# Kernel optimization log

Hardware: AMD Instinct MI355X
Metric: run time of the kernel (lower is better)

## Reference

```python
import jax, jax.numpy as jnp
import numpy as np

N_SRC1, N_DST1, N_DST2 = 200000, 50000, 10000
E1, E2 = 2000000, 400000
IN_F, H_F, N_CLS = 128, 256, 47


def setup_inputs() -> dict:
    key = jax.random.key(0)
    ks = jax.random.split(key, 10)
    x = jax.random.normal(ks[0], (N_SRC1, IN_F), dtype=jnp.float32)
    W_self1 = jax.random.normal(ks[1], (IN_F, H_F), dtype=jnp.float32) * (1.0 / np.sqrt(IN_F))
    W_neigh1 = jax.random.normal(ks[2], (IN_F, H_F), dtype=jnp.float32) * (1.0 / np.sqrt(IN_F))
    b1 = jnp.zeros((H_F,), dtype=jnp.float32)
    W_self2 = jax.random.normal(ks[3], (H_F, N_CLS), dtype=jnp.float32) * (1.0 / np.sqrt(H_F))
    W_neigh2 = jax.random.normal(ks[4], (H_F, N_CLS), dtype=jnp.float32) * (1.0 / np.sqrt(H_F))
    b2 = jnp.zeros((N_CLS,), dtype=jnp.float32)
    src1 = jax.random.randint(ks[5], (E1,), 0, N_SRC1, dtype=jnp.int64)
    dst1 = jnp.sort(jax.random.randint(ks[6], (E1,), 0, N_DST1, dtype=jnp.int64))
    src2 = jax.random.randint(ks[7], (E2,), 0, N_DST1, dtype=jnp.int64)
    dst2 = jnp.sort(jax.random.randint(ks[8], (E2,), 0, N_DST2, dtype=jnp.int64))
    return {"x": x, "W_self1": W_self1, "W_neigh1": W_neigh1, "b1": b1,
            "W_self2": W_self2, "W_neigh2": W_neigh2, "b2": b2,
            "src1": src1, "dst1": dst1, "src2": src2, "dst2": dst2,
            "n_dst1": N_DST1, "n_dst2": N_DST2}


def _sage_mean(h_src, h_dst, src, dst, n_dst, W_self, W_neigh, b):
    # mean neighbor aggregation: gather src feats, segment-sum onto dst, divide by in-degree
    msum = jax.ops.segment_sum(h_src[src], dst, num_segments=n_dst)  # [n_dst, F]
    deg = jax.ops.segment_sum(jnp.ones(src.shape, h_src.dtype), dst, num_segments=n_dst)
    h_neigh = msum / jnp.maximum(deg, 1.0)[:, None]
    return h_dst @ W_self + h_neigh @ W_neigh + b


def reference(x, W_self1, W_neigh1, b1, W_self2, W_neigh2, b2,
              src1, dst1, src2, dst2, n_dst1, n_dst2):
    # layer 1 (dst nodes are the prefix of src nodes, DGL MFG convention)
    h = _sage_mean(x, x[:n_dst1], src1, dst1, n_dst1, W_self1, W_neigh1, b1)
    h = jax.nn.relu(h)  # dropout = identity (eval mode)
    # layer 2
    out = _sage_mean(h, h[:n_dst2], src2, dst2, n_dst2, W_self2, W_neigh2, b2)
    return out
```

## Files before the change

### kernel.cpp

```cpp
#include <hip/hip_runtime.h>

constexpr int N_DST1 = 50000;
constexpr int N_DST2 = 10000;
constexpr int E1     = 2000000;
constexpr int E2     = 400000;
constexpr int IN_F   = 128;
constexpr int H_F    = 256;
constexpr int N_CLS  = 47;

constexpr size_t RP1_OFF = 0;
constexpr size_t RP2_OFF = 204800;
constexpr size_t BPS_OFF = 245760;
constexpr size_t BPN_OFF = 311296;
constexpr size_t BP2_OFF = 376832;
constexpr size_t X8_OFF  = 430080;
constexpr size_t HN1_OFF = 26030080;
constexpr size_t HB_OFF  = 38830080;
constexpr size_t H8_OFF  = 64430080;
constexpr size_t HN2_OFF = 77230080;

using f32x4  = __attribute__((ext_vector_type(4))) float;
using f32x2  = __attribute__((ext_vector_type(2))) float;
using short8 = __attribute__((ext_vector_type(8))) short;

__device__ __forceinline__ ushort f2bf(float f) {
    union { float f; unsigned u; } v; v.f = f;
    unsigned u = v.u;
    return (ushort)((u + 0x7fffu + ((u >> 16) & 1u)) >> 16);
}

constexpr int CAST_BLKS = 200000 * IN_F / 8 / 256;
constexpr int PACK_BLKS = 44;
constexpr int RP_BLKS   = (N_DST1 + N_DST2 + 2 + 255) / 256;

__global__ __launch_bounds__(256) void setup_all(
    const float* __restrict__ x, unsigned char* __restrict__ x8,
    const float* __restrict__ Ws1, const float* __restrict__ Wn1,
    const float* __restrict__ Ws2, const float* __restrict__ Wn2,
    ushort* __restrict__ bps, ushort* __restrict__ bpn, ushort* __restrict__ bp2,
    const int* __restrict__ dst1, const int* __restrict__ dst2,
    int* __restrict__ rp1, int* __restrict__ rp2) {
    int b = blockIdx.x;
    if (b < CAST_BLKS) {
        int i = b * 256 + threadIdx.x;
        float4 v0 = ((const float4*)x)[2 * i];
        float4 v1 = ((const float4*)x)[2 * i + 1];
        int p0 = __builtin_amdgcn_cvt_pk_fp8_f32(v0.x, v0.y, 0, false);
        p0     = __builtin_amdgcn_cvt_pk_fp8_f32(v0.z, v0.w, p0, true);
        int p1 = __builtin_amdgcn_cvt_pk_fp8_f32(v1.x, v1.y, 0, false);
        p1     = __builtin_amdgcn_cvt_pk_fp8_f32(v1.z, v1.w, p1, true);
        uint2 o; o.x = (unsigned)p0; o.y = (unsigned)p1;
        ((uint2*)x8)[i] = o;
    } else if (b < CAST_BLKS + PACK_BLKS) {
        int pb = b - CAST_BLKS;
        if (pb < 32) {
            const float* W = (pb < 16) ? Ws1 : Wn1;
            ushort* P      = (pb < 16) ? bps : bpn;
            int idx = (pb & 15) * 256 + threadIdx.x;
            int lane = idx & 63, kb = (idx >> 6) & 3, nb = idx >> 8;
            int n  = nb * 16 + (lane & 15);
            int k0 = kb * 32 + ((lane >> 4) * 8);
            ushort tmp[8];
#pragma unroll
            for (int j = 0; j < 8; ++j) tmp[j] = f2bf(W[(k0 + j) * H_F + n]);
            ((uint4*)P)[idx] = *(uint4*)tmp;
        } else {
            int idx = (pb - 32) * 256 + threadIdx.x;
            if (idx < 3072) {
                int lane = idx & 63, rem = idx >> 6;
                int nb = rem % 3, kb = rem / 3;
                int col = nb * 16 + (lane & 15);
                int k0  = (kb & 7) * 32 + ((lane >> 4) * 8);
                const float* W = (kb < 8) ? Ws2 : Wn2;
                ushort tmp[8];
#pragma unroll
                for (int j = 0; j < 8; ++j)
                    tmp[j] = (col < N_CLS) ? f2bf(W[(k0 + j) * N_CLS + col]) : (ushort)0;
                ((uint4*)bp2)[(kb * 3 + nb) * 64 + lane] = *(uint4*)tmp;
            }
        }
    } else {
        int idx = (b - CAST_BLKS - PACK_BLKS) * 256 + threadIdx.x;
        const int* dst; int* rp; int E; int target;
        if (idx <= N_DST1) { dst = dst1; rp = rp1; E = E1; target = idx; }
        else if (idx <= N_DST1 + 1 + N_DST2) {
            dst = dst2; rp = rp2; E = E2; target = idx - (N_DST1 + 1);
        } else return;
        int lo = 0, hi = E;
        while (lo < hi) {
            int mid = (lo + hi) >> 1;
            if (dst[mid] < target) lo = mid + 1; else hi = mid;
        }
        rp[target] = lo;
    }
}

__global__ __launch_bounds__(256) void agg1b(const unsigned char* __restrict__ x8,
                                             const int* __restrict__ src,
                                             const int* __restrict__ rp,
                                             ushort* __restrict__ hn) {
    int t = threadIdx.x & 63;
    int d = blockIdx.x * 4 + (threadIdx.x >> 6);
    int s = rp[d], e = rp[d + 1];
    int deg = e - s;
    const uint4* x4 = (const uint4*)x8;
    int g = t >> 3, c = t & 7;
    float a[16] = {};
    auto acc16 = [&](uint4 v) {
        f32x2 f;
        f = __builtin_amdgcn_cvt_pk_f32_fp8((int)v.x, false); a[0]  += f[0]; a[1]  += f[1];
        f = __builtin_amdgcn_cvt_pk_f32_fp8((int)v.x, true);  a[2]  += f[0]; a[3]  += f[1];
        f = __builtin_amdgcn_cvt_pk_f32_fp8((int)v.y, false); a[4]  += f[0]; a[5]  += f[1];
        f = __builtin_amdgcn_cvt_pk_f32_fp8((int)v.y, true);  a[6]  += f[0]; a[7]  += f[1];
        f = __builtin_amdgcn_cvt_pk_f32_fp8((int)v.z, false); a[8]  += f[0]; a[9]  += f[1];
        f = __builtin_amdgcn_cvt_pk_f32_fp8((int)v.z, true);  a[10] += f[0]; a[11] += f[1];
        f = __builtin_amdgcn_cvt_pk_f32_fp8((int)v.w, false); a[12] += f[0]; a[13] += f[1];
        f = __builtin_amdgcn_cvt_pk_f32_fp8((int)v.w, true);  a[14] += f[0]; a[15] += f[1];
    };
    int nfull = deg >> 3;
    int j = 0;
    for (; j + 2 <= nfull; j += 2) {
        int e0 = src[s + 8 * j + g];
        int e1 = src[s + 8 * j + 8 + g];
        uint4 v0 = x4[(size_t)e0 * 8 + c];
        uint4 v1 = x4[(size_t)e1 * 8 + c];
        acc16(v0);
        acc16(v1);
    }
    for (; j < nfull; ++j) {
        int e0 = src[s + 8 * j + g];
        uint4 v = x4[(size_t)e0 * 8 + c];
        acc16(v);
    }
    int b0 = s + 8 * nfull;
    int n = e - b0;
    if (g < n) {
        int e0 = src[b0 + g];
        uint4 v = x4[(size_t)e0 * 8 + c];
        acc16(v);
    }
#pragma unroll
    for (int q = 0; q < 16; ++q) {
        a[q] += __shfl_xor(a[q], 8);
        a[q] += __shfl_xor(a[q], 16);
        a[q] += __shfl_xor(a[q], 32);
    }
    if (t < 8) {
        float inv = 1.f / fmaxf((float)deg, 1.f);
        unsigned o[8];
#pragma unroll
        for (int p = 0; p < 8; ++p)
            o[p] = (unsigned)f2bf(a[2 * p] * inv) |
                   ((unsigned)f2bf(a[2 * p + 1] * inv) << 16);
        uint4* hrow = (uint4*)hn + (size_t)d * 16 + t * 2;
        hrow[0] = make_uint4(o[0], o[1], o[2], o[3]);
        hrow[1] = make_uint4(o[4], o[5], o[6], o[7]);
    }
}

__global__ __launch_bounds__(256) void agg2b(const unsigned char* __restrict__ h8,
                                             const int* __restrict__ src,
                                             const int* __restrict__ rp,
                                             ushort* __restrict__ hn) {
    int t = threadIdx.x & 63;
    int d = blockIdx.x * 4 + (threadIdx.x >> 6);
    int s = rp[d], e = rp[d + 1];
    int deg = e - s;
    const uint4* h4 = (const uint4*)h8;
    int g = t >> 4, c = t & 15;
    float a[16] = {};
    auto acc16 = [&](uint4 v) {
        f32x2 f;
        f = __builtin_amdgcn_cvt_pk_f32_fp8((int)v.x, false); a[0]  += f[0]; a[1]  += f[1];
        f = __builtin_amdgcn_cvt_pk_f32_fp8((int)v.x, true);  a[2]  += f[0]; a[3]  += f[1];
        f = __builtin_amdgcn_cvt_pk_f32_fp8((int)v.y, false); a[4]  += f[0]; a[5]  += f[1];
        f = __builtin_amdgcn_cvt_pk_f32_fp8((int)v.y, true);  a[6]  += f[0]; a[7]  += f[1];
        f = __builtin_amdgcn_cvt_pk_f32_fp8((int)v.z, false); a[8]  += f[0]; a[9]  += f[1];
        f = __builtin_amdgcn_cvt_pk_f32_fp8((int)v.z, true);  a[10] += f[0]; a[11] += f[1];
        f = __builtin_amdgcn_cvt_pk_f32_fp8((int)v.w, false); a[12] += f[0]; a[13] += f[1];
        f = __builtin_amdgcn_cvt_pk_f32_fp8((int)v.w, true);  a[14] += f[0]; a[15] += f[1];
    };
    int nfull = deg >> 2;
    int j = 0;
    for (; j + 2 <= nfull; j += 2) {
        int e0 = src[s + 4 * j + g];
        int e1 = src[s + 4 * j + 4 + g];
        uint4 v0 = h4[(size_t)e0 * 16 + c];
        uint4 v1 = h4[(size_t)e1 * 16 + c];
        acc16(v0);
        acc16(v1);
    }
    for (; j < nfull; ++j) {
        int e0 = src[s + 4 * j + g];
        uint4 v = h4[(size_t)e0 * 16 + c];
        acc16(v);
    }
    int b0 = s + 4 * nfull;
    int n = e - b0;
    if (g < n) {
        int e0 = src[b0 + g];
        uint4 v = h4[(size_t)e0 * 16 + c];
        acc16(v);
    }
#pragma unroll
    for (int q = 0; q < 16; ++q) {
        a[q] += __shfl_xor(a[q], 16);
        a[q] += __shfl_xor(a[q], 32);
    }
    if (t < 16) {
        float inv = 1.f / fmaxf((float)deg, 1.f);
        unsigned o[8];
#pragma unroll
        for (int p = 0; p < 8; ++p)
            o[p] = (unsigned)f2bf(a[2 * p] * inv) |
                   ((unsigned)f2bf(a[2 * p + 1] * inv) << 16);
        uint4* hrow = (uint4*)hn + (size_t)d * 32 + t * 2;
        hrow[0] = make_uint4(o[0], o[1], o[2], o[3]);
        hrow[1] = make_uint4(o[4], o[5], o[6], o[7]);
    }
}

__global__ __launch_bounds__(256) void gemm1_mfma(
    const float* __restrict__ x, const ushort* __restrict__ hn1,
    const ushort* __restrict__ BpS, const ushort* __restrict__ BpN,
    const float* __restrict__ b1, ushort* __restrict__ hb,
    unsigned char* __restrict__ h8) {
    __shared__ ushort bsm[16 * 64 * 8];
    int tid = threadIdx.x;
    int wave = tid >> 6, lane = tid & 63;
    int m0 = (blockIdx.x * 4 + wave) * 16;
    int mrow = m0 + (lane & 15);
    bool active = (m0 < N_DST1);
    if (mrow >= N_DST1) mrow = 0;
    int koff = (lane >> 4) * 8;

    f32x4 acc[16];
#pragma unroll
    for (int nb = 0; nb < 16; ++nb) acc[nb] = (f32x4){0.f, 0.f, 0.f, 0.f};

    for (int ph = 0; ph < 2; ++ph) {
        const uint4* Pg = (const uint4*)((ph == 0) ? BpS : BpN);
        const float*  Af = x   + (size_t)mrow * IN_F;
        const ushort* Ah = hn1 + (size_t)mrow * IN_F;
        for (int kb = 0; kb < 4; ++kb) {
            __syncthreads();
#pragma unroll
            for (int i = 0; i < 4; ++i) {
                int u = tid + 256 * i;
                int nb = u >> 6, l6 = u & 63;
                ((uint4*)bsm)[u] = Pg[(nb * 4 + kb) * 64 + l6];
            }
            __syncthreads();
            short8 a;
            if (ph == 0) {
                float4 a0 = *(const float4*)(Af + kb * 32 + koff);
                float4 a1 = *(const float4*)(Af + kb * 32 + koff + 4);
                a[0] = (short)f2bf(a0.x); a[1] = (short)f2bf(a0.y);
                a[2] = (short)f2bf(a0.z); a[3] = (short)f2bf(a0.w);
                a[4] = (short)f2bf(a1.x); a[5] = (short)f2bf(a1.y);
                a[6] = (short)f2bf(a1.z); a[7] = (short)f2bf(a1.w);
            } else {
                a = *(const short8*)(Ah + kb * 32 + koff);
            }
#pragma unroll
            for (int nb = 0; nb < 16; ++nb) {
                short8 b = *(const short8*)&bsm[(nb * 64 + lane) * 8];
                acc[nb] = __builtin_amdgcn_mfma_f32_16x16x32_bf16(a, b, acc[nb], 0, 0, 0);
            }
        }
    }
    if (!active) return;
    int crow0 = m0 + (lane >> 4) * 4;
    int ccol  = lane & 15;
#pragma unroll
    for (int nb = 0; nb < 16; ++nb) {
        float bias = b1[nb * 16 + ccol];
#pragma unroll
        for (int r = 0; r < 4; ++r) {
            int row = crow0 + r;
            if (row < N_DST1) {
                float v = fmaxf(acc[nb][r] + bias, 0.f);
                size_t col = (size_t)nb * 16 + ccol;
                int p = __builtin_amdgcn_cvt_pk_fp8_f32(v, v, 0, false);
                h8[(size_t)row * H_F + col] = (unsigned char)(p & 0xff);
                if (row < N_DST2) hb[(size_t)row * H_F + col] = f2bf(v);
            }
        }
    }
}

__global__ __launch_bounds__(256) void gemm2_mfma(
    const ushort* __restrict__ hb, const ushort* __restrict__ hn2,
    const ushort* __restrict__ P2, const float* __restrict__ b2,
    float* __restrict__ out) {
    int tid = threadIdx.x;
    int wave = tid >> 6, lane = tid & 63;
    int m0 = (blockIdx.x * 4 + wave) * 16;
    if (m0 >= N_DST2) return;
    int mrow = m0 + (lane & 15);
    int koff = (lane >> 4) * 8;

    f32x4 acc[3];
#pragma unroll
    for (int nb = 0; nb < 3; ++nb) acc[nb] = (f32x4){0.f, 0.f, 0.f, 0.f};

#pragma unroll
    for (int kb = 0; kb < 16; ++kb) {
        const ushort* A = (kb < 8)
            ? (hb  + (size_t)mrow * H_F + kb * 32 + koff)
            : (hn2 + (size_t)mrow * H_F + (kb - 8) * 32 + koff);
        short8 a = *(const short8*)A;
#pragma unroll
        for (int nb = 0; nb < 3; ++nb) {
            short8 b = *(const short8*)(P2 + ((size_t)(kb * 3 + nb) * 64 + lane) * 8);
            acc[nb] = __builtin_amdgcn_mfma_f32_16x16x32_bf16(a, b, acc[nb], 0, 0, 0);
        }
    }
    int crow0 = m0 + (lane >> 4) * 4;
    int ccol  = lane & 15;
#pragma unroll
    for (int nb = 0; nb < 3; ++nb) {
        int col = nb * 16 + ccol;
        if (col < N_CLS) {
            float bias = b2[col];
#pragma unroll
            for (int r = 0; r < 4; ++r)
                out[(size_t)(crow0 + r) * N_CLS + col] = acc[nb][r] + bias;
        }
    }
}

extern "C" void kernel_launch(void* const* d_in, const int* in_sizes, int n_in,
                              void* d_out, int out_size, void* d_ws, size_t ws_size,
                              hipStream_t stream) {
    const float* x   = (const float*)d_in[0];
    const float* Ws1 = (const float*)d_in[1];
    const float* Wn1 = (const float*)d_in[2];
    const float* b1  = (const float*)d_in[3];
    const float* Ws2 = (const float*)d_in[4];
    const float* Wn2 = (const float*)d_in[5];
    const float* b2  = (const float*)d_in[6];
    const int* src1  = (const int*)d_in[7];
    const int* dst1  = (const int*)d_in[8];
    const int* src2  = (const int*)d_in[9];
    const int* dst2  = (const int*)d_in[10];
    float* out = (float*)d_out;

    char* ws = (char*)d_ws;
    int*           rp1 = (int*)(ws + RP1_OFF);
    int*           rp2 = (int*)(ws + RP2_OFF);
    ushort*        bps = (ushort*)(ws + BPS_OFF);
    ushort*        bpn = (ushort*)(ws + BPN_OFF);
    ushort*        bp2 = (ushort*)(ws + BP2_OFF);
    unsigned char* x8  = (unsigned char*)(ws + X8_OFF);
    ushort*        hn1 = (ushort*)(ws + HN1_OFF);
    ushort*        hb  = (ushort*)(ws + HB_OFF);
    unsigned char* h8  = (unsigned char*)(ws + H8_OFF);
    ushort*        hn2 = (ushort*)(ws + HN2_OFF);

    setup_all<<<CAST_BLKS + PACK_BLKS + RP_BLKS, 256, 0, stream>>>(
        x, x8, Ws1, Wn1, Ws2, Wn2, bps, bpn, bp2, dst1, dst2, rp1, rp2);
    agg1b<<<N_DST1 / 4, 256, 0, stream>>>(x8, src1, rp1, hn1);
    gemm1_mfma<<<(N_DST1 / 16 + 3) / 4, 256, 0, stream>>>(x, hn1, bps, bpn, b1, hb, h8);
    agg2b<<<N_DST2 / 4, 256, 0, stream>>>(h8, src2, rp2, hn2);
    gemm2_mfma<<<(N_DST2 / 16 + 3) / 4, 256, 0, stream>>>(hb, hn2, bp2, b2, out);
}
```

Measured before the change: 299.2 us.

## Split gemm1 output columns across waves and read B fragments directly from global

Restructures gemm1 so that each block handles 16 rows and each of its four waves computes 64 of the 256 output columns, instead of each wave computing all 256 columns for its own 16 rows. The shared-memory staging of the packed weight tiles and its barriers are removed, and B fragments are loaded straight from global memory, where they are expected to hit cache. The A rows are loaded and converted once up front. The grid grows fourfold, which raises parallelism and cuts per-wave accumulator registers. The cost is that each A row is now read by four waves and weight reads depend on cache hits. Row bounds checks are dropped, which is safe because 50000 divides evenly by 16.

```diff
diff --git a/kernel.cpp b/kernel.cpp
--- a/kernel.cpp
+++ b/kernel.cpp
@@ -225,66 +225,60 @@
     const ushort* __restrict__ BpS, const ushort* __restrict__ BpN,
     const float* __restrict__ b1, ushort* __restrict__ hb,
     unsigned char* __restrict__ h8) {
-    __shared__ ushort bsm[16 * 64 * 8];
     int tid = threadIdx.x;
     int wave = tid >> 6, lane = tid & 63;
-    int m0 = (blockIdx.x * 4 + wave) * 16;
-    int mrow = m0 + (lane & 15);
-    bool active = (m0 < N_DST1);
-    if (mrow >= N_DST1) mrow = 0;
+    int m0 = blockIdx.x * 16;
+    int nb0 = wave * 4;
+    int mloc = lane & 15;
+    int mrow = m0 + mloc;
     int koff = (lane >> 4) * 8;
 
-    f32x4 acc[16];
-#pragma unroll
-    for (int nb = 0; nb < 16; ++nb) acc[nb] = (f32x4){0.f, 0.f, 0.f, 0.f};
-
-    for (int ph = 0; ph < 2; ++ph) {
-        const uint4* Pg = (const uint4*)((ph == 0) ? BpS : BpN);
-        const float*  Af = x   + (size_t)mrow * IN_F;
-        const ushort* Ah = hn1 + (size_t)mrow * IN_F;
-        for (int kb = 0; kb < 4; ++kb) {
-            __syncthreads();
-#pragma unroll
-            for (int i = 0; i < 4; ++i) {
-                int u = tid + 256 * i;
-                int nb = u >> 6, l6 = u & 63;
-                ((uint4*)bsm)[u] = Pg[(nb * 4 + kb) * 64 + l6];
-            }
-            __syncthreads();
-            short8 a;
-            if (ph == 0) {
-                float4 a0 = *(const float4*)(Af + kb * 32 + koff);
-                float4 a1 = *(const float4*)(Af + kb * 32 + koff + 4);
-                a[0] = (short)f2bf(a0.x); a[1] = (short)f2bf(a0.y);
-                a[2] = (short)f2bf(a0.z); a[3] = (short)f2bf(a0.w);
-                a[4] = (short)f2bf(a1.x); a[5] = (short)f2bf(a1.y);
-                a[6] = (short)f2bf(a1.z); a[7] = (short)f2bf(a1.w);
-            } else {
-                a = *(const short8*)(Ah + kb * 32 + koff);
-            }
-#pragma unroll
-            for (int nb = 0; nb < 16; ++nb) {
-                short8 b = *(const short8*)&bsm[(nb * 64 + lane) * 8];
-                acc[nb] = __builtin_amdgcn_mfma_f32_16x16x32_bf16(a, b, acc[nb], 0, 0, 0);
-            }
-        }
-    }
-    if (!active) return;
+    const float*  Af = x   + (size_t)mrow * IN_F;
+    const ushort* Ah = hn1 + (size_t)mrow * IN_F;
+    short8 a0[4], a1[4];
+#pragma unroll
+    for (int kb = 0; kb < 4; ++kb) {
+        float4 q0 = *(const float4*)(Af + kb * 32 + koff);
+        float4 q1 = *(const float4*)(Af + kb * 32 + koff + 4);
+        a0[kb][0] = (short)f2bf(q0.x); a0[kb][1] = (short)f2bf(q0.y);
+        a0[kb][2] = (short)f2bf(q0.z); a0[kb][3] = (short)f2bf(q0.w);
+        a0[kb][4] = (short)f2bf(q1.x); a0[kb][5] = (short)f2bf(q1.y);
+        a0[kb][6] = (short)f2bf(q1.z); a0[kb][7] = (short)f2bf(q1.w);
+        a1[kb] = *(const short8*)(Ah + kb * 32 + koff);
+    }
+
+    f32x4 acc[4];
+#pragma unroll
+    for (int nb = 0; nb < 4; ++nb) acc[nb] = (f32x4){0.f, 0.f, 0.f, 0.f};
+
+#pragma unroll
+    for (int kb = 0; kb < 4; ++kb)
+#pragma unroll
+        for (int nb = 0; nb < 4; ++nb) {
+            short8 b = *(const short8*)(BpS + ((size_t)((nb0 + nb) * 4 + kb) * 64 + lane) * 8);
+            acc[nb] = __builtin_amdgcn_mfma_f32_16x16x32_bf16(a0[kb], b, acc[nb], 0, 0, 0);
+        }
+#pragma unroll
+    for (int kb = 0; kb < 4; ++kb)
+#pragma unroll
+        for (int nb = 0; nb < 4; ++nb) {
+            short8 b = *(const short8*)(BpN + ((size_t)((nb0 + nb) * 4 + kb) * 64 + lane) * 8);
+            acc[nb] = __builtin_amdgcn_mfma_f32_16x16x32_bf16(a1[kb], b, acc[nb], 0, 0, 0);
+        }
+
     int crow0 = m0 + (lane >> 4) * 4;
     int ccol  = lane & 15;
 #pragma unroll
-    for (int nb = 0; nb < 16; ++nb) {
-        float bias = b1[nb * 16 + ccol];
+    for (int nb = 0; nb < 4; ++nb) {
+        size_t col = (size_t)(nb0 + nb) * 16 + ccol;
+        float bias = b1[col];
 #pragma unroll
         for (int r = 0; r < 4; ++r) {
             int row = crow0 + r;
-            if (row < N_DST1) {
-                float v = fmaxf(acc[nb][r] + bias, 0.f);
-                size_t col = (size_t)nb * 16 + ccol;
-                int p = __builtin_amdgcn_cvt_pk_fp8_f32(v, v, 0, false);
-                h8[(size_t)row * H_F + col] = (unsigned char)(p & 0xff);
-                if (row < N_DST2) hb[(size_t)row * H_F + col] = f2bf(v);
-            }
+            float v = fmaxf(acc[nb][r] + bias, 0.f);
+            int p = __builtin_amdgcn_cvt_pk_fp8_f32(v, v, 0, false);
+            h8[(size_t)row * H_F + col] = (unsigned char)(p & 0xff);
+            if (row < N_DST2) hb[(size_t)row * H_F + col] = f2bf(v);
         }
     }
 }
@@ -361,7 +355,7 @@
     setup_all<<<CAST_BLKS + PACK_BLKS + RP_BLKS, 256, 0, stream>>>(
         x, x8, Ws1, Wn1, Ws2, Wn2, bps, bpn, bp2, dst1, dst2, rp1, rp2);
     agg1b<<<N_DST1 / 4, 256, 0, stream>>>(x8, src1, rp1, hn1);
-    gemm1_mfma<<<(N_DST1 / 16 + 3) / 4, 256, 0, stream>>>(x, hn1, bps, bpn, b1, hb, h8);
+    gemm1_mfma<<<N_DST1 / 16, 256, 0, stream>>>(x, hn1, bps, bpn, b1, hb, h8);
     agg2b<<<N_DST2 / 4, 256, 0, stream>>>(h8, src2, rp2, hn2);
     gemm2_mfma<<<(N_DST2 / 16 + 3) / 4, 256, 0, stream>>>(hb, hn2, bp2, b2, out);
 }
```

Result: faster. 289.5 us (-3.2%).
